# Kernel tuning notes

Measured on AMD Instinct MI355X. Metric: run time of the kernel, lower is better.

The kernel has to match this reference:

```python
import jax, jax.numpy as jnp
import numpy as np

B_, H_, W_, C_ = 8, 56, 56, 96
D_ = int(C_ * 2.0)          # d_inner = 192
N_ = 16                     # d_state
K_ = 4                      # scan directions
R_ = (C_ + 15) // 16        # dt_rank 'auto' = 6
MLP_H = 4 * C_
EPS = 1e-5


def setup_inputs() -> dict:
    key = jax.random.key(0)
    ks = jax.random.split(key, 16)
    s = 0.02
    rn = lambda k, sh, sc=1.0: jax.random.normal(k, sh, dtype=jnp.float32) * sc
    return dict(
        x=rn(ks[0], (B_, H_, W_, C_)),
        ln1_w=jnp.ones((C_,), jnp.float32), ln1_b=jnp.zeros((C_,), jnp.float32),
        in_proj_w=rn(ks[1], (2 * D_, C_), s),
        conv_w=rn(ks[2], (D_, 1, 3, 3), s), conv_b=jnp.zeros((D_,), jnp.float32),
        x_proj_w=rn(ks[3], (K_, R_ + 2 * N_, D_), s),
        dt_proj_w=rn(ks[4], (K_, D_, R_), s),
        dt_proj_b=rn(ks[5], (K_, D_), 0.1),
        A_logs=jax.random.uniform(ks[6], (K_ * D_, N_), jnp.float32, 0.0, 3.0),
        Ds=jnp.ones((K_ * D_,), jnp.float32),
        out_norm_w=jnp.ones((D_,), jnp.float32), out_norm_b=jnp.zeros((D_,), jnp.float32),
        out_proj_w=rn(ks[7], (C_, D_), s),
        ln2_w=jnp.ones((C_,), jnp.float32), ln2_b=jnp.zeros((C_,), jnp.float32),
        fc1_w=rn(ks[8], (MLP_H, C_), s), fc1_b=jnp.zeros((MLP_H,), jnp.float32),
        fc2_w=rn(ks[9], (C_, MLP_H), s), fc2_b=jnp.zeros((C_,), jnp.float32),
    )


def layer_norm(x, w, b):
    m = x.mean(-1, keepdims=True)
    v = ((x - m) ** 2).mean(-1, keepdims=True)
    return (x - m) / jnp.sqrt(v + EPS) * w + b


def ss2d(x, in_proj_w, conv_w, conv_b, x_proj_w, dt_proj_w, dt_proj_b,
         A_logs, Ds, out_norm_w, out_norm_b, out_proj_w):
    Bn, Hh, Ww, C = x.shape
    L = Hh * Ww
    xz = x @ in_proj_w.T                       # (B,H,W,2D)
    xc, z = jnp.split(xz, 2, axis=-1)
    xc = xc.transpose(0, 3, 1, 2)              # (B,D,H,W)
    xc = jax.lax.conv_general_dilated(xc, conv_w, (1, 1), 'SAME',
                                      feature_group_count=D_)
    xc = jax.nn.silu(xc + conv_b[None, :, None, None])
    # cross-scan: 4 traversal orders, each (B,D,L)
    x0 = xc.reshape(Bn, D_, L)
    x1 = xc.transpose(0, 1, 3, 2).reshape(Bn, D_, L)
    xs = jnp.stack([x0, x1, x0[..., ::-1], x1[..., ::-1]], axis=1)  # (B,K,D,L)
    xdbl = jnp.einsum('bkdl,kcd->bkcl', xs, x_proj_w)
    dts, Bs, Cs = jnp.split(xdbl, [R_, R_ + N_], axis=2)            # (B,K,R,L),(B,K,N,L)x2
    dts = jnp.einsum('bkrl,kdr->bkdl', dts, dt_proj_w)
    dts = jax.nn.softplus(dts + dt_proj_b[None, :, :, None])        # (B,K,D,L)
    A = -jnp.exp(A_logs).reshape(K_, D_, N_)                        # (K,D,N)

    def step(h, inp):
        xt, dtt, Bt, Ct = inp                  # (B,K,D),(B,K,D),(B,K,N),(B,K,N)
        h = h * jnp.exp(dtt[..., None] * A) + (dtt * xt)[..., None] * Bt[:, :, None, :]
        return h, jnp.einsum('bkdn,bkn->bkd', h, Ct)

    inps = (xs.transpose(3, 0, 1, 2), dts.transpose(3, 0, 1, 2),
            Bs.transpose(3, 0, 1, 2), Cs.transpose(3, 0, 1, 2))
    h0 = jnp.zeros((Bn, K_, D_, N_), jnp.float32)
    _, ys = jax.lax.scan(step, h0, inps)       # (L,B,K,D)
    ys = ys.transpose(1, 2, 3, 0)              # (B,K,D,L)
    ys = ys + Ds.reshape(K_, D_)[None, :, :, None] * xs
    # cross-merge: undo flips and transposed order
    y = ys[:, 0] + ys[:, 2, :, ::-1]
    y = y + (ys[:, 1] + ys[:, 3, :, ::-1]).reshape(Bn, D_, Ww, Hh) \
            .transpose(0, 1, 3, 2).reshape(Bn, D_, L)
    y = y.transpose(0, 2, 1).reshape(Bn, Hh, Ww, D_)
    y = layer_norm(y, out_norm_w, out_norm_b)
    y = y * jax.nn.silu(z)
    return y @ out_proj_w.T


def reference(x, ln1_w, ln1_b, in_proj_w, conv_w, conv_b, x_proj_w, dt_proj_w,
              dt_proj_b, A_logs, Ds, out_norm_w, out_norm_b, out_proj_w,
              ln2_w, ln2_b, fc1_w, fc1_b, fc2_w, fc2_b):
    # norm -> SS2D -> residual
    x = x + ss2d(layer_norm(x, ln1_w, ln1_b), in_proj_w, conv_w, conv_b,
                 x_proj_w, dt_proj_w, dt_proj_b, A_logs, Ds,
                 out_norm_w, out_norm_b, out_proj_w)
    # norm -> MLP -> residual
    h = layer_norm(x, ln2_w, ln2_b)
    h = jax.nn.gelu(h @ fc1_w.T + fc1_b) @ fc2_w.T + fc2_b
    return x + h
```

## Files before the change

### kernel.cpp

```cpp
#include <hip/hip_runtime.h>
#include <hip/hip_bf16.h>

typedef __hip_bfloat16 bf16;
typedef short bf16x8 __attribute__((ext_vector_type(8)));
typedef float f32x4 __attribute__((ext_vector_type(4)));

#define BBATCH 8
#define HHH 56
#define WWW 56
#define CCH 96
#define DIN 192
#define NST 16
#define KDIR 4
#define RDT 6
#define LLEN 3136
#define BLTOT 25088
#define SSEG 112
#define SEGL 28
#define PJC 38
#define PJW 152
#define PJS 40
#define PJS1 24
#define MLPH 384

#if defined(__has_builtin)
#if __has_builtin(__builtin_amdgcn_exp2f)
#define EXP2F(x) __builtin_amdgcn_exp2f(x)
#endif
#if __has_builtin(__builtin_amdgcn_logf)
#define LOG2F_(x) __builtin_amdgcn_logf(x)
#endif
#endif
#ifndef EXP2F
#define EXP2F(x) __expf((x) * 0.69314718056f)
#endif
#ifndef LOG2F_
#define LOG2F_(x) (__logf(x) * 1.44269504f)
#endif
#define LOG2E 1.44269504f

__device__ __forceinline__ float2 pk_mul(float2 a, float2 b) {
    float2 d;
    asm("v_pk_mul_f32 %0, %1, %2" : "=v"(d) : "v"(a), "v"(b));
    return d;
}
__device__ __forceinline__ float2 pk_fma(float2 a, float2 b, float2 c) {
    float2 d;
    asm("v_pk_fma_f32 %0, %1, %2, %3" : "=v"(d) : "v"(a), "v"(b), "v"(c));
    return d;
}

__device__ __forceinline__ float b2f(bf16 v) { return __bfloat162float(v); }
__device__ __forceinline__ bf16  f2b(float v) { return __float2bfloat16(v); }
__device__ __forceinline__ unsigned short f2bu(float f) {
    union { bf16 h; unsigned short u; } c; c.h = __float2bfloat16(f); return c.u;
}
__device__ __forceinline__ float bu2f(unsigned short u) {
    union { unsigned short u; bf16 h; } c; c.u = u; return __bfloat162float(c.h);
}
__device__ __forceinline__ float sigm(float x) { return 1.f / (1.f + __expf(-x)); }
__device__ __forceinline__ float softplusf(float x) {
    float t = EXP2F(-fabsf(x) * LOG2E);
    return fmaxf(x, 0.f) + 0.69314718f * LOG2F_(1.f + t);
}
__device__ __forceinline__ float geluf(float v) {
    float u = 0.7978845608028654f * (v + 0.044715f * v * v * v);
    float ey = __expf(2.f * u);
    float th = 1.f - 2.f / (ey + 1.f);
    return 0.5f * v * (1.f + th);
}

__device__ __forceinline__ int pos_map(int k, int l) {
    if (k & 2) l = LLEN - 1 - l;
    if (k & 1) { int q = l / WWW; int r = l - q * WWW; return r * WWW + q; }
    return l;
}

__global__ __launch_bounds__(256) void k0_pre(
    const float* __restrict__ Alog, float* __restrict__ a2g) {
    int i = blockIdx.x * 256 + threadIdx.x;
    a2g[i] = -__expf(Alog[i]) * LOG2E;
}

__global__ __launch_bounds__(256) void k0w(
    const float* __restrict__ w1, const float* __restrict__ w2,
    const float* __restrict__ w3, const float* __restrict__ w4,
    const float* __restrict__ w5, unsigned short* __restrict__ o) {
    int i = blockIdx.x * 256 + threadIdx.x;
    float v;
    if (i < 36864)       v = w1[i];
    else if (i < 66048)  v = w2[i - 36864];
    else if (i < 84480)  v = w3[i - 66048];
    else if (i < 121344) v = w4[i - 84480];
    else                 v = w5[i - 121344];
    o[i] = f2bu(v);
}

template<int N, int K, int EPI, bool LNIN>
__global__ __launch_bounds__(256) void gemm_mfma(
    const void* __restrict__ Xv, const unsigned short* __restrict__ Wb,
    const float* __restrict__ bias, const float* __restrict__ res,
    const float* __restrict__ lnw, const float* __restrict__ lnb,
    void* __restrict__ out0v, void* __restrict__ out1v) {
    __shared__ unsigned short a_sh[128 * 40];
    __shared__ unsigned short b_sh[64 * 40];
    __shared__ float mrow[128], rrow[128];
    __shared__ float lnw_sh[96], lnb_sh[96];
    const int t = threadIdx.x;
    const int P0 = blockIdx.x * 128;
    const int N0 = blockIdx.y * 64;
    const int w = t >> 6, lane = t & 63, q = lane >> 4, nl = lane & 15;
    if constexpr (LNIN) {
        const float* Xf = (const float*)Xv;
        const float* xr = Xf + (size_t)(P0 + (t >> 1)) * 96 + (t & 1) * 48;
        float s = 0.f, s2 = 0.f;
#pragma unroll
        for (int i = 0; i < 12; ++i) {
            float4 v = *(const float4*)&xr[i * 4];
            s += v.x + v.y + v.z + v.w;
            s2 += v.x * v.x + v.y * v.y + v.z * v.z + v.w * v.w;
        }
        s += __shfl_xor(s, 1); s2 += __shfl_xor(s2, 1);
        if ((t & 1) == 0) {
            float m = s * (1.f / 96.f);
            float var = s2 * (1.f / 96.f) - m * m;
            mrow[t >> 1] = m; rrow[t >> 1] = rsqrtf(var + 1e-5f);
        }
        if (t < 96) { lnw_sh[t] = lnw[t]; lnb_sh[t] = lnb[t]; }
    }
    f32x4 acc[2][4];
#pragma unroll
    for (int i = 0; i < 2; ++i)
#pragma unroll
        for (int j = 0; j < 4; ++j)
            acc[i][j] = (f32x4){0.f, 0.f, 0.f, 0.f};
    for (int k0 = 0; k0 < K; k0 += 32) {
        __syncthreads();
#pragma unroll
        for (int it = 0; it < 2; ++it) {
            int idx = t + it * 256;
            int pr = idx >> 2, kq = idx & 3;
            if constexpr (LNIN) {
                const float* Xf = (const float*)Xv;
                const float* src = &Xf[(size_t)(P0 + pr) * K + k0 + kq * 8];
                float m = mrow[pr], r = rrow[pr];
                float4 v0 = *(const float4*)src;
                float4 v1 = *(const float4*)(src + 4);
                int c0 = k0 + kq * 8;
                ushort4 u0, u1;
                u0.x = f2bu((v0.x - m) * r * lnw_sh[c0+0] + lnb_sh[c0+0]);
                u0.y = f2bu((v0.y - m) * r * lnw_sh[c0+1] + lnb_sh[c0+1]);
                u0.z = f2bu((v0.z - m) * r * lnw_sh[c0+2] + lnb_sh[c0+2]);
                u0.w = f2bu((v0.w - m) * r * lnw_sh[c0+3] + lnb_sh[c0+3]);
                u1.x = f2bu((v1.x - m) * r * lnw_sh[c0+4] + lnb_sh[c0+4]);
                u1.y = f2bu((v1.y - m) * r * lnw_sh[c0+5] + lnb_sh[c0+5]);
                u1.z = f2bu((v1.z - m) * r * lnw_sh[c0+6] + lnb_sh[c0+6]);
                u1.w = f2bu((v1.w - m) * r * lnw_sh[c0+7] + lnb_sh[c0+7]);
                *(ushort4*)&a_sh[pr * 40 + kq * 8] = u0;
                *(ushort4*)&a_sh[pr * 40 + kq * 8 + 4] = u1;
            } else {
                const unsigned short* X = (const unsigned short*)Xv;
                uint4 v = *(const uint4*)&X[(size_t)(P0 + pr) * K + k0 + kq * 8];
                *(uint4*)&a_sh[pr * 40 + kq * 8] = v;
            }
        }
        {
            int nr = t >> 2, kq = t & 3;
            int ng = N0 + nr; if (ng > N - 1) ng = N - 1;
            uint4 v = *(const uint4*)&Wb[(size_t)ng * K + k0 + kq * 8];
            *(uint4*)&b_sh[nr * 40 + kq * 8] = v;
        }
        __syncthreads();
        bf16x8 af[2], bfr[4];
#pragma unroll
        for (int mf = 0; mf < 2; ++mf)
            af[mf] = *(const bf16x8*)&a_sh[(w * 32 + mf * 16 + nl) * 40 + q * 8];
#pragma unroll
        for (int nf = 0; nf < 4; ++nf)
            bfr[nf] = *(const bf16x8*)&b_sh[(nf * 16 + nl) * 40 + q * 8];
#pragma unroll
        for (int mf = 0; mf < 2; ++mf)
#pragma unroll
            for (int nf = 0; nf < 4; ++nf)
                acc[mf][nf] = __builtin_amdgcn_mfma_f32_16x16x32_bf16(
                    af[mf], bfr[nf], acc[mf][nf], 0, 0, 0);
    }
#pragma unroll
    for (int mf = 0; mf < 2; ++mf) {
#pragma unroll
        for (int nf = 0; nf < 4; ++nf) {
#pragma unroll
            for (int r = 0; r < 4; ++r) {
                float v = acc[mf][nf][r];
                size_t pos = (size_t)P0 + w * 32 + mf * 16 + q * 4 + r;
                int n = N0 + nf * 16 + nl;
                if constexpr (EPI == 0) {
                    unsigned short* xc = (unsigned short*)out0v;
                    unsigned short* zz = (unsigned short*)out1v;
                    if (n < 192) xc[pos * 192 + n] = f2bu(v);
                    else         zz[pos * 192 + (n - 192)] = f2bu(v);
                } else if constexpr (EPI == 1) {
                    if (n < 152) ((float*)out0v)[pos * 152 + n] = v;
                } else if constexpr (EPI == 2) {
                    if (n < 96) ((float*)out0v)[pos * 96 + n] = res[pos * 96 + n] + v;
                } else if constexpr (EPI == 3) {
                    ((unsigned short*)out0v)[pos * 384 + n] = f2bu(geluf(v + bias[n]));
                } else {
                    if (n < 96) ((float*)out0v)[pos * 96 + n] =
                        res[pos * 96 + n] + bias[n] + v;
                }
            }
        }
    }
}

__global__ __launch_bounds__(256) void k2_conv(
    const unsigned short* __restrict__ xcpre, const float* __restrict__ cw,
    const float* __restrict__ cb, unsigned short* __restrict__ xconv) {
    int idx = blockIdx.x * 256 + threadIdx.x;
    int dd = idx % 48;
    int P = idx / 48;
    int d0 = dd * 4;
    int b = P / LLEN, l = P - b * LLEN;
    int h = l / WWW, w = l - h * WWW;
    float acc0 = cb[d0], acc1 = cb[d0 + 1], acc2 = cb[d0 + 2], acc3 = cb[d0 + 3];
#pragma unroll
    for (int i = 0; i < 3; ++i) {
        int hh = h + i - 1;
        if (hh < 0 || hh >= HHH) continue;
#pragma unroll
        for (int j = 0; j < 3; ++j) {
            int ww = w + j - 1;
            if (ww < 0 || ww >= WWW) continue;
            ushort4 xv = *(const ushort4*)&xcpre[
                ((size_t)(b * LLEN + hh * WWW + ww)) * DIN + d0];
            acc0 = fmaf(bu2f(xv.x), cw[(d0 + 0) * 9 + i * 3 + j], acc0);
            acc1 = fmaf(bu2f(xv.y), cw[(d0 + 1) * 9 + i * 3 + j], acc1);
            acc2 = fmaf(bu2f(xv.z), cw[(d0 + 2) * 9 + i * 3 + j], acc2);
            acc3 = fmaf(bu2f(xv.w), cw[(d0 + 3) * 9 + i * 3 + j], acc3);
        }
    }
    acc0 = acc0 * sigm(acc0); acc1 = acc1 * sigm(acc1);
    acc2 = acc2 * sigm(acc2); acc3 = acc3 * sigm(acc3);
    ushort4 o;
    o.x = f2bu(acc0); o.y = f2bu(acc1); o.z = f2bu(acc2); o.w = f2bu(acc3);
    *(ushort4*)&xconv[(size_t)P * DIN + d0] = o;
}

__global__ __launch_bounds__(192) void k4_scan1(
    const bf16* __restrict__ xconv, const float* __restrict__ proj,
    const float* __restrict__ dtw, const float* __restrict__ dtb,
    const float* __restrict__ a2g, float* __restrict__ hloc,
    float* __restrict__ tsum) {
    __shared__ float pl[SEGL * PJS1];
    __shared__ int posl[SEGL];
    const int bid = blockIdx.x;
    const int s = bid % SSEG;
    const int bk = bid / SSEG;
    const int k = bk & 3, b = bk >> 2;
    const int d = threadIdx.x;
    const int l0 = s * SEGL;
    for (int q = d; q < SEGL * 22; q += 192) {
        int st = q / 22, c = q - st * 22;
        int p = pos_map(k, l0 + st);
        int ofs = (c < 6) ? c : c + 2;
        pl[st * PJS1 + ofs] = proj[(size_t)(b * LLEN + p) * PJW + k * PJC + c];
    }
    if (d < SEGL) posl[d] = pos_map(k, l0 + d) * DIN;
    float w6[RDT];
#pragma unroll
    for (int r = 0; r < RDT; ++r) w6[r] = dtw[(k * DIN + d) * RDT + r];
    const float bias = dtb[k * DIN + d];
    float2 a2[8];
#pragma unroll
    for (int j = 0; j < 8; ++j)
        a2[j] = *(const float2*)&a2g[(k * DIN + d) * NST + 2 * j];
    float2 h2[8];
#pragma unroll
    for (int j = 0; j < 8; ++j) h2[j] = make_float2(0.f, 0.f);
    float T = 0.f;
    __syncthreads();
    const bf16* xg = xconv + (size_t)b * LLEN * DIN + d;
    for (int bt = 0; bt < 4; ++bt) {
        int off7[7]; float xv7[7];
#pragma unroll
        for (int i = 0; i < 7; ++i) off7[i] = posl[bt * 7 + i];
#pragma unroll
        for (int i = 0; i < 7; ++i) xv7[i] = b2f(xg[off7[i]]);
#pragma unroll
        for (int i = 0; i < 7; ++i) {
            const float* rowf = &pl[(bt * 7 + i) * PJS1];
            float4 g0 = *(const float4*)(rowf);
            float2 g1 = *(const float2*)(rowf + 4);
            float dtv = bias;
            dtv = fmaf(g0.x, w6[0], dtv); dtv = fmaf(g0.y, w6[1], dtv);
            dtv = fmaf(g0.z, w6[2], dtv); dtv = fmaf(g0.w, w6[3], dtv);
            dtv = fmaf(g1.x, w6[4], dtv); dtv = fmaf(g1.y, w6[5], dtv);
            dtv = softplusf(dtv);
            T += dtv;
            float2 dt2 = make_float2(dtv, dtv);
            float2 u2 = make_float2(dtv * xv7[i], dtv * xv7[i]);
#pragma unroll
            for (int g = 0; g < 4; ++g) {
                float4 Bv = *(const float4*)(rowf + 8 + 4 * g);
                float2 Blo = make_float2(Bv.x, Bv.y);
                float2 Bhi = make_float2(Bv.z, Bv.w);
                float2 alo = pk_mul(dt2, a2[2 * g]);
                float2 ahi = pk_mul(dt2, a2[2 * g + 1]);
                float2 elo, ehi;
                elo.x = EXP2F(alo.x); elo.y = EXP2F(alo.y);
                ehi.x = EXP2F(ahi.x); ehi.y = EXP2F(ahi.y);
                h2[2 * g]     = pk_fma(h2[2 * g],     elo, pk_mul(u2, Blo));
                h2[2 * g + 1] = pk_fma(h2[2 * g + 1], ehi, pk_mul(u2, Bhi));
            }
        }
    }
    size_t base = ((size_t)bid * DIN + d) * NST;
#pragma unroll
    for (int j = 0; j < 8; ++j) *(float2*)&hloc[base + 2 * j] = h2[j];
    tsum[bid * DIN + d] = T;
}

__global__ __launch_bounds__(256) void k5_carry(
    const float* hloc, const float* __restrict__ tsum,
    const float* __restrict__ a2g, float* hin) {
    int g = blockIdx.x * 256 + threadIdx.x;
    int n = g & 15;
    int dk = g >> 4;
    int d = dk % DIN;
    int bk = dk / DIN;
    int k = bk & 3;
    float a2 = a2g[(k * DIN + d) * NST + n];
    float Hc = 0.f;
    for (int s = 0; s < SSEG; ++s) {
        int bid = bk * SSEG + s;
        size_t idx = ((size_t)bid * DIN + d) * NST + n;
        float hl = hloc[idx];
        float Tv = tsum[bid * DIN + d];
        hin[idx] = Hc;
        Hc = fmaf(EXP2F(a2 * Tv), Hc, hl);
    }
}

__global__ __launch_bounds__(192) void k6_scan2(
    const bf16* __restrict__ xconv, const float* __restrict__ proj,
    const float* __restrict__ dtw, const float* __restrict__ dtb,
    const float* __restrict__ a2g, const float* __restrict__ Dsp,
    const float* __restrict__ hin, bf16* __restrict__ ysm) {
    __shared__ float pl[SEGL * PJS];
    __shared__ int posl[SEGL];
    const int bid = blockIdx.x;
    const int s = bid % SSEG;
    const int bk = bid / SSEG;
    const int k = bk & 3, b = bk >> 2;
    const int d = threadIdx.x;
    const int l0 = s * SEGL;
    for (int q = d; q < SEGL * PJC; q += 192) {
        int st = q / PJC, c = q - st * PJC;
        int p = pos_map(k, l0 + st);
        int ofs = (c < 6) ? c : c + 2;
        pl[st * PJS + ofs] = proj[(size_t)(b * LLEN + p) * PJW + k * PJC + c];
    }
    if (d < SEGL) posl[d] = pos_map(k, l0 + d) * DIN;
    float w6[RDT];
#pragma unroll
    for (int r = 0; r < RDT; ++r) w6[r] = dtw[(k * DIN + d) * RDT + r];
    const float bias = dtb[k * DIN + d];
    const float dsv = Dsp[k * DIN + d];
    float2 a2[8];
#pragma unroll
    for (int j = 0; j < 8; ++j)
        a2[j] = *(const float2*)&a2g[(k * DIN + d) * NST + 2 * j];
    float2 h2[8];
    size_t hbase = ((size_t)bid * DIN + d) * NST;
#pragma unroll
    for (int j = 0; j < 8; ++j) h2[j] = *(const float2*)&hin[hbase + 2 * j];
    __syncthreads();
    const bf16* xg = xconv + (size_t)b * LLEN * DIN + d;
    bf16* ysg = ysm + ((size_t)bk * LLEN) * DIN + d;
    for (int bt = 0; bt < 4; ++bt) {
        int off7[7]; float xv7[7];
#pragma unroll
        for (int i = 0; i < 7; ++i) off7[i] = posl[bt * 7 + i];
#pragma unroll
        for (int i = 0; i < 7; ++i) xv7[i] = b2f(xg[off7[i]]);
#pragma unroll
        for (int i = 0; i < 7; ++i) {
            const float* rowf = &pl[(bt * 7 + i) * PJS];
            float4 g0 = *(const float4*)(rowf);
            float2 g1 = *(const float2*)(rowf + 4);
            float dtv = bias;
            dtv = fmaf(g0.x, w6[0], dtv); dtv = fmaf(g0.y, w6[1], dtv);
            dtv = fmaf(g0.z, w6[2], dtv); dtv = fmaf(g0.w, w6[3], dtv);
            dtv = fmaf(g1.x, w6[4], dtv); dtv = fmaf(g1.y, w6[5], dtv);
            dtv = softplusf(dtv);
            float2 dt2 = make_float2(dtv, dtv);
            float2 u2 = make_float2(dtv * xv7[i], dtv * xv7[i]);
            float2 yac0 = make_float2(0.f, 0.f), yac1 = make_float2(0.f, 0.f);
#pragma unroll
            for (int g = 0; g < 4; ++g) {
                float4 Bv = *(const float4*)(rowf + 8 + 4 * g);
                float4 Cv = *(const float4*)(rowf + 24 + 4 * g);
                float2 Blo = make_float2(Bv.x, Bv.y);
                float2 Bhi = make_float2(Bv.z, Bv.w);
                float2 Clo = make_float2(Cv.x, Cv.y);
                float2 Chi = make_float2(Cv.z, Cv.w);
                float2 alo = pk_mul(dt2, a2[2 * g]);
                float2 ahi = pk_mul(dt2, a2[2 * g + 1]);
                float2 elo, ehi;
                elo.x = EXP2F(alo.x); elo.y = EXP2F(alo.y);
                ehi.x = EXP2F(ahi.x); ehi.y = EXP2F(ahi.y);
                h2[2 * g]     = pk_fma(h2[2 * g],     elo, pk_mul(u2, Blo));
                h2[2 * g + 1] = pk_fma(h2[2 * g + 1], ehi, pk_mul(u2, Bhi));
                yac0 = pk_fma(h2[2 * g],     Clo, yac0);
                yac1 = pk_fma(h2[2 * g + 1], Chi, yac1);
            }
            float y = (yac0.x + yac0.y) + (yac1.x + yac1.y);
            ysg[off7[i]] = f2b(fmaf(dsv, xv7[i], y));
        }
    }
}

__global__ __launch_bounds__(256) void k65_merge(
    const bf16* __restrict__ ysm, const bf16* __restrict__ z,
    const float* __restrict__ onw, const float* __restrict__ onb,
    bf16* __restrict__ ymod) {
    __shared__ float rb[16 * DIN];
    __shared__ float ps[256], pq[256];
    __shared__ float mrow[16], srow[16];
    const int t = threadIdx.x;
    const int P0 = blockIdx.x * 16;
    for (int q = t; q < 16 * DIN; q += 256) {
        int pos = q / DIN, c = q - pos * DIN;
        int P = P0 + pos;
        int b = P / LLEN, l = P - b * LLEN;
        size_t base = ((size_t)(b * KDIR) * LLEN + l) * DIN + c;
        size_t pstr = (size_t)LLEN * DIN;
        float v = b2f(ysm[base]) + b2f(ysm[base + pstr]) +
                  b2f(ysm[base + 2 * pstr]) + b2f(ysm[base + 3 * pstr]);
        rb[q] = v;
    }
    __syncthreads();
    {
        int pos = t >> 4, part = t & 15;
        float s = 0.f, s2 = 0.f;
        for (int i = 0; i < 12; ++i) {
            float v = rb[pos * DIN + part * 12 + i];
            s += v; s2 += v * v;
        }
        ps[pos * 16 + part] = s; pq[pos * 16 + part] = s2;
    }
    __syncthreads();
    if (t < 16) {
        float s = 0.f, s2 = 0.f;
        for (int i = 0; i < 16; ++i) { s += ps[t * 16 + i]; s2 += pq[t * 16 + i]; }
        float m = s * (1.f / DIN);
        float v = s2 * (1.f / DIN) - m * m;
        mrow[t] = m; srow[t] = rsqrtf(v + 1e-5f);
    }
    __syncthreads();
    for (int q = t; q < 16 * DIN; q += 256) {
        int pos = q / DIN, c = q - pos * DIN;
        int P = P0 + pos;
        float v = (rb[q] - mrow[pos]) * srow[pos] * onw[c] + onb[c];
        float zv = b2f(z[(size_t)P * DIN + c]);
        v *= zv * sigm(zv);
        ymod[(size_t)P * DIN + c] = f2b(v);
    }
}

extern "C" void kernel_launch(void* const* d_in, const int* in_sizes, int n_in,
                              void* d_out, int out_size, void* d_ws, size_t ws_size,
                              hipStream_t stream) {
    const float* x      = (const float*)d_in[0];
    const float* ln1w   = (const float*)d_in[1];
    const float* ln1b   = (const float*)d_in[2];
    const float* inpW   = (const float*)d_in[3];
    const float* convW  = (const float*)d_in[4];
    const float* convB  = (const float*)d_in[5];
    const float* xprojW = (const float*)d_in[6];
    const float* dtW    = (const float*)d_in[7];
    const float* dtB    = (const float*)d_in[8];
    const float* Alog   = (const float*)d_in[9];
    const float* Dsp    = (const float*)d_in[10];
    const float* onw    = (const float*)d_in[11];
    const float* onb    = (const float*)d_in[12];
    const float* outW   = (const float*)d_in[13];
    const float* ln2w   = (const float*)d_in[14];
    const float* ln2b   = (const float*)d_in[15];
    const float* fc1W   = (const float*)d_in[16];
    const float* fc1b   = (const float*)d_in[17];
    const float* fc2W   = (const float*)d_in[18];
    const float* fc2b   = (const float*)d_in[19];
    float* out = (float*)d_out;

    char* ws = (char*)d_ws;
    unsigned short* z_us    = (unsigned short*)(ws + 0);
    bf16*  z_bf             = (bf16*)z_us;
    bf16*  xconv_bf         = (bf16*)(ws + 9633792);
    float* proj_f           = (float*)(ws + 19267584);
    bf16*  ymod_bf          = (bf16*)(ws + 19267584);
    float* tsum_f           = (float*)(ws + 34521088);
    unsigned short* xcpre_us= (unsigned short*)(ws + 39337984);
    float* hloc_f           = (float*)(ws + 39337984);
    float* hin_f            = hloc_f;
    float* y1_f             = (float*)(ws + 39337984);
    bf16*  ysm_bf           = (bf16*)(ws + 83378176);
    unsigned short* hmlp_us = (unsigned short*)(ws + 83378176);
    float* a2g_f            = (float*)(ws + 121913344);
    unsigned short* wbf_us  = (unsigned short*)(ws + 121962496);

    k0_pre<<<48, 256, 0, stream>>>(Alog, a2g_f);
    k0w<<<618, 256, 0, stream>>>(inpW, xprojW, outW, fc1W, fc2W, wbf_us);
    gemm_mfma<384, 96, 0, true><<<dim3(196, 6), 256, 0, stream>>>(
        x, wbf_us + 0, nullptr, nullptr, ln1w, ln1b, xcpre_us, z_us);
    k2_conv<<<4704, 256, 0, stream>>>(xcpre_us, convW, convB,
                                      (unsigned short*)xconv_bf);
    gemm_mfma<152, 192, 1, false><<<dim3(196, 3), 256, 0, stream>>>(
        xconv_bf, wbf_us + 36864, nullptr, nullptr, nullptr, nullptr,
        proj_f, nullptr);
    k4_scan1<<<3584, 192, 0, stream>>>(xconv_bf, proj_f, dtW, dtB, a2g_f,
                                       hloc_f, tsum_f);
    k5_carry<<<384, 256, 0, stream>>>(hloc_f, tsum_f, a2g_f, hin_f);
    k6_scan2<<<3584, 192, 0, stream>>>(xconv_bf, proj_f, dtW, dtB, a2g_f, Dsp,
                                       hin_f, ysm_bf);
    k65_merge<<<1568, 256, 0, stream>>>(ysm_bf, z_bf, onw, onb, ymod_bf);
    gemm_mfma<96, 192, 2, false><<<dim3(196, 2), 256, 0, stream>>>(
        ymod_bf, wbf_us + 66048, nullptr, x, nullptr, nullptr, y1_f, nullptr);
    gemm_mfma<384, 96, 3, true><<<dim3(196, 6), 256, 0, stream>>>(
        y1_f, wbf_us + 84480, fc1b, nullptr, ln2w, ln2b, hmlp_us, nullptr);
    gemm_mfma<96, 384, 4, false><<<dim3(196, 2), 256, 0, stream>>>(
        hmlp_us, wbf_us + 121344, fc2b, y1_f, nullptr, nullptr, out, nullptr);
}
```

Baseline: 370.1 us.

## Load GEMM operands directly into MFMA registers, dropping shared-memory staging

Reworks the bf16 MFMA GEMM so each lane loads its A and B fragments straight from global memory into registers instead of staging tiles through LDS with two barriers per K step. The fused LayerNorm input path now computes row statistics per lane with cross-lane shuffles, keeps the full 96-wide row in registers, and reads ln weights directly. This removes LDS traffic and synchronisation, but each warp now fetches the weight tile separately and loads are narrower and less coalesced. The K loop is fully unrolled, which raises register use.

Result: slower. 391.4 us (+5.8%).

```diff
diff --git a/kernel.cpp b/kernel.cpp
--- a/kernel.cpp
+++ b/kernel.cpp
@@ -102,88 +102,98 @@
     const float* __restrict__ bias, const float* __restrict__ res,
     const float* __restrict__ lnw, const float* __restrict__ lnb,
     void* __restrict__ out0v, void* __restrict__ out1v) {
-    __shared__ unsigned short a_sh[128 * 40];
-    __shared__ unsigned short b_sh[64 * 40];
-    __shared__ float mrow[128], rrow[128];
-    __shared__ float lnw_sh[96], lnb_sh[96];
     const int t = threadIdx.x;
     const int P0 = blockIdx.x * 128;
     const int N0 = blockIdx.y * 64;
     const int w = t >> 6, lane = t & 63, q = lane >> 4, nl = lane & 15;
+    f32x4 acc[2][4];
+#pragma unroll
+    for (int i = 0; i < 2; ++i)
+#pragma unroll
+        for (int j = 0; j < 4; ++j)
+            acc[i][j] = (f32x4){0.f, 0.f, 0.f, 0.f};
+
+    const unsigned short* bp[4];
+#pragma unroll
+    for (int nf = 0; nf < 4; ++nf) {
+        int ng = N0 + nf * 16 + nl; if (ng > N - 1) ng = N - 1;
+        bp[nf] = &Wb[(size_t)ng * K + q * 8];
+    }
+
     if constexpr (LNIN) {
         const float* Xf = (const float*)Xv;
-        const float* xr = Xf + (size_t)(P0 + (t >> 1)) * 96 + (t & 1) * 48;
-        float s = 0.f, s2 = 0.f;
-#pragma unroll
-        for (int i = 0; i < 12; ++i) {
-            float4 v = *(const float4*)&xr[i * 4];
-            s += v.x + v.y + v.z + v.w;
-            s2 += v.x * v.x + v.y * v.y + v.z * v.z + v.w * v.w;
-        }
-        s += __shfl_xor(s, 1); s2 += __shfl_xor(s2, 1);
-        if ((t & 1) == 0) {
+        float av[2][3][8];
+        float mv[2], rv[2];
+#pragma unroll
+        for (int mf = 0; mf < 2; ++mf) {
+            const float* rp = Xf + (size_t)(P0 + w * 32 + mf * 16 + nl) * 96 + q * 8;
+            float s = 0.f, s2 = 0.f;
+#pragma unroll
+            for (int it = 0; it < 3; ++it) {
+                float4 v0 = *(const float4*)(rp + it * 32);
+                float4 v1 = *(const float4*)(rp + it * 32 + 4);
+                av[mf][it][0] = v0.x; av[mf][it][1] = v0.y;
+                av[mf][it][2] = v0.z; av[mf][it][3] = v0.w;
+                av[mf][it][4] = v1.x; av[mf][it][5] = v1.y;
+                av[mf][it][6] = v1.z; av[mf][it][7] = v1.w;
+                s += v0.x + v0.y + v0.z + v0.w + v1.x + v1.y + v1.z + v1.w;
+                s2 += v0.x * v0.x + v0.y * v0.y + v0.z * v0.z + v0.w * v0.w +
+                      v1.x * v1.x + v1.y * v1.y + v1.z * v1.z + v1.w * v1.w;
+            }
+            s += __shfl_xor(s, 16); s2 += __shfl_xor(s2, 16);
+            s += __shfl_xor(s, 32); s2 += __shfl_xor(s2, 32);
             float m = s * (1.f / 96.f);
             float var = s2 * (1.f / 96.f) - m * m;
-            mrow[t >> 1] = m; rrow[t >> 1] = rsqrtf(var + 1e-5f);
-        }
-        if (t < 96) { lnw_sh[t] = lnw[t]; lnb_sh[t] = lnb[t]; }
-    }
-    f32x4 acc[2][4];
-#pragma unroll
-    for (int i = 0; i < 2; ++i)
-#pragma unroll
-        for (int j = 0; j < 4; ++j)
-            acc[i][j] = (f32x4){0.f, 0.f, 0.f, 0.f};
-    for (int k0 = 0; k0 < K; k0 += 32) {
-        __syncthreads();
-#pragma unroll
-        for (int it = 0; it < 2; ++it) {
-            int idx = t + it * 256;
-            int pr = idx >> 2, kq = idx & 3;
-            if constexpr (LNIN) {
-                const float* Xf = (const float*)Xv;
-                const float* src = &Xf[(size_t)(P0 + pr) * K + k0 + kq * 8];
-                float m = mrow[pr], r = rrow[pr];
-                float4 v0 = *(const float4*)src;
-                float4 v1 = *(const float4*)(src + 4);
-                int c0 = k0 + kq * 8;
-                ushort4 u0, u1;
-                u0.x = f2bu((v0.x - m) * r * lnw_sh[c0+0] + lnb_sh[c0+0]);
-                u0.y = f2bu((v0.y - m) * r * lnw_sh[c0+1] + lnb_sh[c0+1]);
-                u0.z = f2bu((v0.z - m) * r * lnw_sh[c0+2] + lnb_sh[c0+2]);
-                u0.w = f2bu((v0.w - m) * r * lnw_sh[c0+3] + lnb_sh[c0+3]);
-                u1.x = f2bu((v1.x - m) * r * lnw_sh[c0+4] + lnb_sh[c0+4]);
-                u1.y = f2bu((v1.y - m) * r * lnw_sh[c0+5] + lnb_sh[c0+5]);
-                u1.z = f2bu((v1.z - m) * r * lnw_sh[c0+6] + lnb_sh[c0+6]);
-                u1.w = f2bu((v1.w - m) * r * lnw_sh[c0+7] + lnb_sh[c0+7]);
-                *(ushort4*)&a_sh[pr * 40 + kq * 8] = u0;
-                *(ushort4*)&a_sh[pr * 40 + kq * 8 + 4] = u1;
-            } else {
-                const unsigned short* X = (const unsigned short*)Xv;
-                uint4 v = *(const uint4*)&X[(size_t)(P0 + pr) * K + k0 + kq * 8];
-                *(uint4*)&a_sh[pr * 40 + kq * 8] = v;
-            }
-        }
-        {
-            int nr = t >> 2, kq = t & 3;
-            int ng = N0 + nr; if (ng > N - 1) ng = N - 1;
-            uint4 v = *(const uint4*)&Wb[(size_t)ng * K + k0 + kq * 8];
-            *(uint4*)&b_sh[nr * 40 + kq * 8] = v;
-        }
-        __syncthreads();
-        bf16x8 af[2], bfr[4];
+            mv[mf] = m; rv[mf] = rsqrtf(var + 1e-5f);
+        }
+#pragma unroll
+        for (int it = 0; it < 3; ++it) {
+            int c0 = it * 32 + q * 8;
+            float4 w0 = *(const float4*)&lnw[c0];
+            float4 w1 = *(const float4*)&lnw[c0 + 4];
+            float4 b0 = *(const float4*)&lnb[c0];
+            float4 b1 = *(const float4*)&lnb[c0 + 4];
+            float wj[8] = {w0.x, w0.y, w0.z, w0.w, w1.x, w1.y, w1.z, w1.w};
+            float bj[8] = {b0.x, b0.y, b0.z, b0.w, b1.x, b1.y, b1.z, b1.w};
+            bf16x8 af[2], bfr[4];
+#pragma unroll
+            for (int mf = 0; mf < 2; ++mf)
+#pragma unroll
+                for (int j = 0; j < 8; ++j)
+                    af[mf][j] = (short)f2bu(
+                        (av[mf][it][j] - mv[mf]) * rv[mf] * wj[j] + bj[j]);
+#pragma unroll
+            for (int nf = 0; nf < 4; ++nf)
+                bfr[nf] = *(const bf16x8*)(bp[nf] + it * 32);
+#pragma unroll
+            for (int mf = 0; mf < 2; ++mf)
+#pragma unroll
+                for (int nf = 0; nf < 4; ++nf)
+                    acc[mf][nf] = __builtin_amdgcn_mfma_f32_16x16x32_bf16(
+                        af[mf], bfr[nf], acc[mf][nf], 0, 0, 0);
+        }
+    } else {
+        const unsigned short* X = (const unsigned short*)Xv;
+        const unsigned short* ap[2];
 #pragma unroll
         for (int mf = 0; mf < 2; ++mf)
-            af[mf] = *(const bf16x8*)&a_sh[(w * 32 + mf * 16 + nl) * 40 + q * 8];
-#pragma unroll
-        for (int nf = 0; nf < 4; ++nf)
-            bfr[nf] = *(const bf16x8*)&b_sh[(nf * 16 + nl) * 40 + q * 8];
-#pragma unroll
-        for (int mf = 0; mf < 2; ++mf)
+            ap[mf] = &X[(size_t)(P0 + w * 32 + mf * 16 + nl) * K + q * 8];
+#pragma unroll
+        for (int it = 0; it < K / 32; ++it) {
+            bf16x8 af[2], bfr[4];
+#pragma unroll
+            for (int mf = 0; mf < 2; ++mf)
+                af[mf] = *(const bf16x8*)(ap[mf] + it * 32);
 #pragma unroll
             for (int nf = 0; nf < 4; ++nf)
-                acc[mf][nf] = __builtin_amdgcn_mfma_f32_16x16x32_bf16(
-                    af[mf], bfr[nf], acc[mf][nf], 0, 0, 0);
+                bfr[nf] = *(const bf16x8*)(bp[nf] + it * 32);
+#pragma unroll
+            for (int mf = 0; mf < 2; ++mf)
+#pragma unroll
+                for (int nf = 0; nf < 4; ++nf)
+                    acc[mf][nf] = __builtin_amdgcn_mfma_f32_16x16x32_bf16(
+                        af[mf], bfr[nf], acc[mf][nf], 0, 0, 0);
+        }
     }
 #pragma unroll
     for (int mf = 0; mf < 2; ++mf) {
```
